# Performance work log

Hardware: AMD Instinct MI355X
Metric: run time of the kernel (lower is better)

## Reference

```python
import jax, jax.numpy as jnp
import numpy as np

NUM_QUERIES = 256
NUM_NEGATIVES = 512
NUM_GENERALIZED = 8
GEN_RADIUS = 1.0
TEMP = 0.5
STRONG_THRESHOLD = 0.97


def _mls(mu0, mu1, s0, s1):
    # mutual likelihood score; mu's are L2-normalized (F.normalize, eps=1e-12)
    mu0 = mu0 / jnp.maximum(jnp.linalg.norm(mu0, axis=-1, keepdims=True), 1e-12)
    mu1 = mu1 / jnp.maximum(jnp.linalg.norm(mu1, axis=-1, keepdims=True), 1e-12)
    down = s0 + s1
    return -0.5 * (((mu0 - mu1) ** 2) / down + jnp.log(down)).mean(-1)


def setup_inputs() -> dict:
    key = jax.random.key(0)
    B, S, H, W, C = 4, 19, 128, 128, 256
    ks = jax.random.split(key, 6)
    mu = jax.random.normal(ks[0], (B, C, H, W), jnp.float32)
    sigma = jax.random.uniform(ks[1], (B, C, H, W), jnp.float32, minval=0.1, maxval=1.0)
    cls = jax.random.randint(ks[2], (B, H, W), 0, S)
    label = jnp.transpose(jax.nn.one_hot(cls, S, dtype=jnp.float32), (0, 3, 1, 2))  # [B,S,H,W]
    mask = jnp.ones((B, 1, H, W), jnp.float32)
    prob = jax.random.uniform(ks[3], (B, S, H, W), jnp.float32)
    mmt_prototype_mu = jax.random.normal(ks[4], (S, 1, C), jnp.float32)
    mmt_prototype_sigma = jax.random.uniform(ks[5], (S, 1, C), jnp.float32, minval=0.1, maxval=1.0)
    return {"mu": mu, "sigma": sigma, "label": label, "mask": mask, "prob": prob,
            "mmt_prototype_mu": mmt_prototype_mu, "mmt_prototype_sigma": mmt_prototype_sigma,
            "epoch": 0, "iter_i": 0}


def reference(mu, sigma, label, mask, prob, mmt_prototype_mu, mmt_prototype_sigma, epoch, iter_i):
    B, C, H, W = mu.shape
    S = label.shape[1]
    P = B * H * W
    Q, NEG, G = NUM_QUERIES, NUM_NEGATIVES, NUM_GENERALIZED
    key = jax.random.key(1234)

    valid = (label * mask).transpose(1, 0, 2, 3).reshape(S, P)            # [S,P] float
    mu_f = mu.transpose(0, 2, 3, 1).reshape(P, C)                          # [P,C]
    sg_f = sigma.transpose(0, 2, 3, 1).reshape(P, C)
    prob_f = prob.transpose(1, 0, 2, 3).reshape(S, P)
    hard = (prob_f < STRONG_THRESHOLD).astype(valid.dtype) * valid         # [S,P]

    # --- segment prototypes (precision-weighted fusion), detached as in torch.no_grad ---
    inv_sg = 1.0 / sg_f
    proto_sigma_b = 1.0 / jnp.einsum('sp,pc->sc', valid, inv_sg)           # [S,C]
    proto_mu_b = proto_sigma_b * jnp.einsum('sp,pc->sc', valid, inv_sg * mu_f)
    mmt_mu = mmt_prototype_mu[:, 0, :]
    mmt_sg = mmt_prototype_sigma[:, 0, :]
    proto_sigma = 1.0 / (1.0 / proto_sigma_b + 1.0 / mmt_sg)               # momentum fusion
    proto_mu = proto_sigma * (mmt_mu / mmt_sg + proto_mu_b / proto_sigma_b)
    proto_mu = jax.lax.stop_gradient(proto_mu)
    proto_sigma = jax.lax.stop_gradient(proto_sigma)

    # cumulative masks for uniform sampling over valid / hard pixels via searchsorted
    valid_cum = jnp.cumsum(valid, axis=1)                                  # [S,P]
    valid_cnt = valid_cum[:, -1]
    hard_cum = jnp.cumsum(hard, axis=1)
    hard_cnt = hard_cum[:, -1]

    loss = jnp.float32(0.0)
    for i in range(S):
        ki = jax.random.fold_in(key, i)
        k_anc, k_cls, k_neg, k_gen = jax.random.split(ki, 4)
        # anchors: uniform over hard pixels of segment i
        u = jax.random.uniform(k_anc, (Q,)) * hard_cnt[i]
        a_idx = jnp.clip(jnp.searchsorted(hard_cum[i], u, side='right'), 0, P - 1)
        anchor_mu = mu_f[a_idx]                                            # [Q,C]
        anchor_sg = sg_f[a_idx]
        # negative class distribution from prototype MLS similarity
        others = jnp.concatenate([jnp.arange(i + 1, S), jnp.arange(0, i)])  # [S-1]
        sim = _mls(proto_mu[i][None], proto_mu[others], proto_sigma[i][None], proto_sigma[others])
        logp = jax.nn.log_softmax(sim / TEMP)
        samp = jax.random.categorical(k_cls, logp, shape=(Q, NEG))          # idx into `others`
        cls_g = others[samp.reshape(-1)]                                    # [Q*NEG] global class
        # uniform pixel within each sampled class (vectorized searchsorted over classes)
        un = jax.random.uniform(k_neg, (Q * NEG,))
        idx_all = jax.vmap(lambda cs, cnt: jnp.searchsorted(cs, un * cnt, side='right'))(valid_cum, valid_cnt)
        n_idx = jnp.clip(idx_all[cls_g, jnp.arange(Q * NEG)], 0, P - 1)
        neg_mu = jax.lax.stop_gradient(mu_f[n_idx].reshape(Q, NEG, C))
        neg_sg = jax.lax.stop_gradient(sg_f[n_idx].reshape(Q, NEG, C))
        pos_mu = jnp.broadcast_to(proto_mu[i][None, None], (Q, 1, C))
        pos_sg = jnp.broadcast_to(proto_sigma[i][None, None], (Q, 1, C))
        # generalized negatives: reparameterized samples from (updated) momentum prototypes
        eps = jax.random.normal(k_gen, (S - 1, G, C))
        gen = proto_mu[others][:, None, :] + GEN_RADIUS * jnp.sqrt(proto_sigma[others])[:, None, :] * eps
        gen = jnp.broadcast_to(gen.reshape(1, (S - 1) * G, C), (Q, (S - 1) * G, C))
        all_mu = jnp.concatenate([pos_mu, neg_mu, gen], axis=1)             # [Q,1+NEG+(S-1)*G,C]
        all_sg = jnp.concatenate([pos_sg, neg_sg, jnp.zeros_like(gen)], axis=1)
        logits = _mls(anchor_mu[:, None, :], all_mu, anchor_sg[:, None, :], all_sg) / TEMP
        loss = loss - jax.nn.log_softmax(logits, axis=-1)[:, 0].mean()      # CE vs target 0
    return loss / S
```

## Files before the change

kernel.cpp:

```cpp
#include <hip/hip_runtime.h>
#include <hip/hip_fp16.h>
#include <hip/hip_fp8.h>
#include <cstdint>

#define B_   4
#define S_   19
#define HW_  16384
#define P_   65536
#define C_   256
#define Q_   256
#define NEG_ 512
#define NS_  131072
#define GENV_ 144
#define NANCH (S_ * 256)
#define NPAIR (NANCH / 2)
#define NBUCK 8

typedef float v2f __attribute__((ext_vector_type(2)));

#if __has_builtin(__builtin_amdgcn_cvt_pk_f32_fp8) && __has_builtin(__builtin_amdgcn_cvt_pk_fp8_f32)
#define HAVE_HW_FP8 1
#endif

template<int W> __device__ __forceinline__ v2f cvt8(uint32_t d) {
#ifdef HAVE_HW_FP8
  v2f r = __builtin_amdgcn_cvt_pk_f32_fp8((int)d, W);
  return r;
#else
  __hip_fp8_e4m3 h0, h1;
  h0.__x = (uint8_t)(d >> (W * 16));
  h1.__x = (uint8_t)(d >> (W * 16 + 8));
  v2f r; r.x = (float)h0; r.y = (float)h1; return r;
#endif
}
template<int W> __device__ __forceinline__ uint32_t pk8(float a, float b, uint32_t old) {
#ifdef HAVE_HW_FP8
  return (uint32_t)__builtin_amdgcn_cvt_pk_fp8_f32(a, b, (int)old, W);
#else
  __hip_fp8_e4m3 ha(a), hb(b);
  uint32_t v = (uint32_t)ha.__x | ((uint32_t)hb.__x << 8);
  return (old & (W ? 0x0000FFFFu : 0xFFFF0000u)) | (v << (W * 16));
#endif
}

__device__ __forceinline__ void tf2x32(uint32_t k0, uint32_t k1, uint32_t x0, uint32_t x1,
                                       uint32_t& o0, uint32_t& o1) {
  uint32_t k2 = k0 ^ k1 ^ 0x1BD11BDAu;
#define TFR(r) { x0 += x1; x1 = (x1 << r) | (x1 >> (32 - r)); x1 ^= x0; }
  x0 += k0; x1 += k1;
  TFR(13) TFR(15) TFR(26) TFR(6)  x0 += k1; x1 += k2 + 1u;
  TFR(17) TFR(29) TFR(16) TFR(24) x0 += k2; x1 += k0 + 2u;
  TFR(13) TFR(15) TFR(26) TFR(6)  x0 += k0; x1 += k1 + 3u;
  TFR(17) TFR(29) TFR(16) TFR(24) x0 += k1; x1 += k2 + 4u;
  TFR(13) TFR(15) TFR(26) TFR(6)  x0 += k2; x1 += k0 + 5u;
#undef TFR
  o0 = x0; o1 = x1;
}

__device__ __forceinline__ uint32_t rbits(uint32_t k0, uint32_t k1, uint32_t n) {
  uint32_t a, b; tf2x32(k0, k1, 0u, n, a, b); return a ^ b;
}

__device__ __forceinline__ float bits2f01(uint32_t b) {
  return __uint_as_float((b >> 9) | 0x3f800000u) - 1.0f;
}

__device__ __forceinline__ float fastrcp(float x) {
  float r; asm("v_rcp_f32 %0, %1" : "=v"(r) : "v"(x)); return r;
}

__device__ __forceinline__ float wred(float v) {
#pragma unroll
  for (int off = 32; off > 0; off >>= 1) v += __shfl_xor(v, off, 64);
  return v;
}
__device__ __forceinline__ void wred3(float& a, float& b, float& c) {
#pragma unroll
  for (int off = 32; off > 0; off >>= 1) {
    a += __shfl_xor(a, off, 64);
    b += __shfl_xor(b, off, 64);
    c += __shfl_xor(c, off, 64);
  }
}

__device__ __forceinline__ void lse_up(float lg, float& m, float& l) {
  if (lg > m) { l = l * __expf(m - lg) + 1.0f; m = lg; }
  else l += __expf(lg - m);
}
__device__ __forceinline__ void lse_merge(float& m, float& l, float mo, float lo) {
  float mn = fmaxf(m, mo);
  l = l * __expf(m - mn) + lo * __expf(mo - mn);
  m = mn;
}

__device__ __forceinline__ float erfinv_f(float x) {
  float w = -__logf(fmaxf(fmaf(-x, x, 1.0f), 1e-37f));
  float p;
  if (w < 5.0f) {
    w -= 2.5f;
    p = 2.81022636e-08f;
    p = fmaf(p, w, 3.43273939e-07f);
    p = fmaf(p, w, -3.5233877e-06f);
    p = fmaf(p, w, -4.39150654e-06f);
    p = fmaf(p, w, 0.00021858087f);
    p = fmaf(p, w, -0.00125372503f);
    p = fmaf(p, w, -0.00417768164f);
    p = fmaf(p, w, 0.246640727f);
    p = fmaf(p, w, 1.50140941f);
  } else {
    w = sqrtf(w) - 3.0f;
    p = -0.000200214257f;
    p = fmaf(p, w, 0.000100950558f);
    p = fmaf(p, w, 0.00134934322f);
    p = fmaf(p, w, -0.00367342844f);
    p = fmaf(p, w, 0.00573950773f);
    p = fmaf(p, w, -0.0076224613f);
    p = fmaf(p, w, 0.00943887047f);
    p = fmaf(p, w, 1.00167406f);
    p = fmaf(p, w, 2.83297682f);
  }
  return p * x;
}

__global__ __launch_bounds__(256) void k_classify(const float* __restrict__ label,
    const float* __restrict__ mask, const float* __restrict__ prob,
    const float* __restrict__ mu,
    uint32_t* __restrict__ keys, int* __restrict__ cls, int* __restrict__ hrd,
    int* __restrict__ bcv, int* __restrict__ bch, float2* __restrict__ rnrm) {
  __shared__ int hv[S_], hh[S_];
  int t = threadIdx.x;
  if (t < S_) { hv[t] = 0; hh[t] = 0; }
  if (blockIdx.x == 0 && t < S_) {
    uint32_t f0, f1;
    tf2x32(0u, 1234u, 0u, (uint32_t)t, f0, f1);
#pragma unroll
    for (int k = 0; k < 4; ++k) {
      uint32_t a, b;
      tf2x32(f0, f1, 0u, (uint32_t)k, a, b);
      keys[t * 8 + k * 2] = a; keys[t * 8 + k * 2 + 1] = b;
    }
  }
  __syncthreads();
  int p = blockIdx.x * 256 + t;
  int b = p >> 14, rem = p & (HW_ - 1);
  int sp = -1;
#pragma unroll
  for (int s = 0; s < S_; ++s) {
    float l = label[((b * S_ + s) << 14) + rem];
    if (l > 0.5f) sp = s;
  }
  if (mask[(b << 14) + rem] <= 0.5f) sp = -1;
  int h = 0;
  if (sp >= 0) h = (prob[((b * S_ + sp) << 14) + rem] < 0.97f) ? 1 : 0;
  cls[p] = sp; hrd[p] = h;
  if (sp >= 0) { atomicAdd(&hv[sp], 1); if (h) atomicAdd(&hh[sp], 1); }
  __syncthreads();
  if (t < S_) { bcv[t * 256 + blockIdx.x] = hv[t]; bch[t * 256 + blockIdx.x] = hh[t]; }
  const float* basep = mu + (((size_t)(b * C_)) << 14) + rem;
  float s2 = 0.f;
#pragma unroll 8
  for (int c = 0; c < C_; ++c) {
    float v = basep[(size_t)c << 14];
    s2 = fmaf(v, v, s2);
  }
  float nrm = sqrtf(s2);
  rnrm[p] = make_float2(fastrcp(fmaxf(nrm, 1e-12f)), nrm);
}

__global__ __launch_bounds__(256) void k_pack(const float* __restrict__ mu,
    const float* __restrict__ sg, const float2* __restrict__ rnrm,
    uint32_t* __restrict__ pair8) {
  __shared__ float smu[64][65];
  __shared__ float ssg[64][65];
  __shared__ float srn[64];
  int p0 = blockIdx.x * 64, c0 = blockIdx.y * 64;
  int b = p0 >> 14, rem0 = p0 & (HW_ - 1);
  if (threadIdx.x < 64) srn[threadIdx.x] = rnrm[p0 + threadIdx.x].x;
  int px = threadIdx.x & 63, cy = threadIdx.x >> 6;
#pragma unroll
  for (int itr = 0; itr < 16; ++itr) {
    int cl = cy + itr * 4;
    int addr = ((b * C_ + c0 + cl) << 14) + rem0 + px;
    smu[cl][px] = mu[addr];
    ssg[cl][px] = sg[addr];
  }
  __syncthreads();
#pragma unroll
  for (int itr = 0; itr < 8; ++itr) {
    int e = itr * 256 + threadIdx.x;
    int pxl = e >> 5, dw = e & 31, cl = dw * 2;
    float rn = srn[pxl];
    uint32_t wd = pk8<0>(smu[cl][pxl] * rn, ssg[cl][pxl], 0u);
    wd = pk8<1>(smu[cl + 1][pxl] * rn, ssg[cl + 1][pxl], wd);
    pair8[(size_t)(p0 + pxl) * 128 + (c0 >> 1) + dw] = wd;
  }
}

__global__ __launch_bounds__(320) void k_scan(const int* __restrict__ bcv, const int* __restrict__ bch,
    int* __restrict__ bov, int* __restrict__ boh,
    int* __restrict__ cntv, int* __restrict__ cnth,
    int* __restrict__ basev, int* __restrict__ baseh) {
  __shared__ int psv[S_][16], psh[S_][16], scv[S_], sch[S_];
  int t = threadIdx.x;
  int s = t >> 4, c = t & 15;
  if (t < 304) {
    int sv = 0, sh = 0;
#pragma unroll 4
    for (int b = 0; b < 16; ++b) {
      sv += bcv[s * 256 + c * 16 + b];
      sh += bch[s * 256 + c * 16 + b];
    }
    psv[s][c] = sv; psh[s][c] = sh;
  }
  __syncthreads();
  if (t < S_) {
    int rv = 0, rh = 0;
#pragma unroll
    for (int cc = 0; cc < 16; ++cc) {
      int tv = psv[t][cc]; psv[t][cc] = rv; rv += tv;
      int th = psh[t][cc]; psh[t][cc] = rh; rh += th;
    }
    cntv[t] = rv; cnth[t] = rh; scv[t] = rv; sch[t] = rh;
  }
  __syncthreads();
  if (t == 0) {
    int bv = 0, bh = 0;
    for (int k = 0; k < S_; ++k) { basev[k] = bv; bv += scv[k]; baseh[k] = bh; bh += sch[k]; }
  }
  if (t < 304) {
    int rv = psv[s][c], rh = psh[s][c];
#pragma unroll 4
    for (int b = 0; b < 16; ++b) {
      int i0 = s * 256 + c * 16 + b;
      int tv = bcv[i0]; bov[i0] = rv; rv += tv;
      int th = bch[i0]; boh[i0] = rh; rh += th;
    }
  }
}

__global__ __launch_bounds__(256) void k_fillsums(const uint32_t* __restrict__ pair8,
    const float2* __restrict__ rnrm, const int* __restrict__ cls, const int* __restrict__ hrd,
    const int* __restrict__ bov, const int* __restrict__ boh,
    const int* __restrict__ basev, const int* __restrict__ baseh,
    int* __restrict__ posv, int* __restrict__ posh, float* __restrict__ part) {
  __shared__ float lacc[S_][2][C_];
  __shared__ int scls[256];
  __shared__ int slh[256];
  __shared__ float snrm[256];
  int t = threadIdx.x;
  int p0 = blockIdx.x * 256;
  int p = p0 + t;
  int s = cls[p]; int h = hrd[p];
  scls[t] = s; slh[t] = h;
  snrm[t] = rnrm[p].y;
  for (int e = t; e < S_ * 2 * C_; e += 256) (&lacc[0][0][0])[e] = 0.f;
  __syncthreads();
  if (s >= 0) {
    int rv = 0, rh = 0;
    for (int k = 0; k < t; ++k) { if (scls[k] == s) { rv++; rh += slh[k]; } }
    posv[basev[s] + bov[s * 256 + blockIdx.x] + rv] = p;
    if (h) posh[baseh[s] + boh[s * 256 + blockIdx.x] + rh] = p;
  }
  int half = t & 1, dwi = t >> 1;
  uint32_t d = pair8[(size_t)p0 * 128 + dwi];
  for (int pp = 0; pp < 256; ++pp) {
    uint32_t dnx = (pp + 1 < 256) ? pair8[(size_t)(p0 + pp + 1) * 128 + dwi] : 0u;
    int sc = scls[pp];
    if (sc >= 0) {
      v2f e = half ? cvt8<1>(d) : cvt8<0>(d);
      float ia = fastrcp(e.y);
      lacc[sc][0][t] += ia;
      lacc[sc][1][t] += ia * e.x * snrm[pp];
    }
    d = dnx;
  }
  __syncthreads();
  float* dst = part + (size_t)blockIdx.x * (2 * S_ * C_);
  for (int e = t; e < S_ * 2 * C_; e += 256) dst[e] = (&lacc[0][0][0])[e];
}

__global__ __launch_bounds__(1024) void k_proto(const float* __restrict__ part,
    const float* __restrict__ mmu, const float* __restrict__ msg,
    float* __restrict__ pmu, float* __restrict__ psig, float* __restrict__ phat) {
  __shared__ float redA[4][C_];
  __shared__ float redB[4][C_];
  __shared__ float red[4];
  int s = blockIdx.x;
  int t = threadIdx.x;
  int c = t & 255, grp = t >> 8;
  float A = 0.f, Bv = 0.f;
  for (int b = grp * 64; b < grp * 64 + 64; ++b) {
    const float* pb = part + (size_t)b * (2 * S_ * C_) + (s * 2) * C_;
    A += pb[c];
    Bv += pb[C_ + c];
  }
  redA[grp][c] = A; redB[grp][c] = Bv;
  __syncthreads();
  float pm = 0.f;
  if (grp == 0) {
    A = redA[0][c] + redA[1][c] + redA[2][c] + redA[3][c];
    Bv = redB[0][c] + redB[1][c] + redB[2][c] + redB[3][c];
    int e = s * C_ + c;
    float psb = 1.0f / A;
    float pmb = psb * Bv;
    float ms = msg[e], mm = mmu[e];
    float ps = 1.0f / (1.0f / psb + 1.0f / ms);
    pm = ps * (mm / ms + pmb / psb);
    pmu[e] = pm; psig[e] = ps;
    float w = wred(pm * pm);
    int lane = c & 63, wv = c >> 6;
    if (lane == 0) red[wv] = w;
  }
  __syncthreads();
  if (grp == 0) {
    float tot = red[0] + red[1] + red[2] + red[3];
    float nrm = fmaxf(sqrtf(tot), 1e-12f);
    phat[s * C_ + c] = pm / nrm;
  }
}

__global__ __launch_bounds__(64) void k_simlogp(const float* __restrict__ phat,
    const float* __restrict__ psig, float* __restrict__ logp) {
  int i = blockIdx.x, lane = threadIdx.x;
  int c0 = lane * 4;
  float phi[4], psi[4];
#pragma unroll
  for (int k = 0; k < 4; ++k) { phi[k] = phat[i * C_ + c0 + k]; psi[k] = psig[i * C_ + c0 + k]; }
  float xs[18];
#pragma unroll
  for (int j = 0; j < 18; ++j) {
    int o = i + 1 + j; if (o >= S_) o -= S_;
    float t = 0.f;
#pragma unroll
    for (int k = 0; k < 4; ++k) {
      float d = phi[k] - phat[o * C_ + c0 + k];
      float dn = psi[k] + psig[o * C_ + c0 + k];
      t += d * d / dn + logf(dn);
    }
    t = wred(t);
    xs[j] = (-0.5f * t * (1.0f / 256.0f)) * 2.0f;
  }
  float m = xs[0];
#pragma unroll
  for (int j = 1; j < 18; ++j) m = fmaxf(m, xs[j]);
  float se = 0.f;
#pragma unroll
  for (int j = 0; j < 18; ++j) se += expf(xs[j] - m);
  float lg = logf(se);
  if (lane == 0) {
#pragma unroll
    for (int j = 0; j < 18; ++j) logp[i * 18 + j] = xs[j] - m - lg;
  }
}

__global__ __launch_bounds__(256) void k_gensample(const uint32_t* __restrict__ keys,
    const float* __restrict__ pmu, const float* __restrict__ psig,
    const float* __restrict__ logp, const int* __restrict__ cntv, const int* __restrict__ basev,
    const int* __restrict__ posv, float* __restrict__ ghat, int* __restrict__ nidx) {
  __shared__ float red[4];
  __shared__ float elp[18];
  __shared__ int lcnt[S_], lbase[S_];
  int bid = blockIdx.x;
  int t = threadIdx.x;
  if (bid < GENV_ * S_) {
    int v = bid % GENV_, i = bid / GENV_;
    int c = t;
    int o = i + 1 + (v >> 3); if (o >= S_) o -= S_;
    uint32_t k0 = keys[i * 8 + 6], k1 = keys[i * 8 + 7];
    uint32_t bits = rbits(k0, k1, (uint32_t)(v * C_ + c));
    float f01 = bits2f01(bits);
    const float lo = -0.99999994f;
    float u = fmaxf(f01 * 2.0f + lo, lo);
    float eps = 1.41421356237f * erfinv_f(u);
    float g = pmu[o * C_ + c] + sqrtf(psig[o * C_ + c]) * eps;
    float w = wred(g * g);
    int lane = c & 63, wv = c >> 6;
    if (lane == 0) red[wv] = w;
    __syncthreads();
    float tot = red[0] + red[1] + red[2] + red[3];
    float nrm = fmaxf(sqrtf(tot), 1e-12f);
    ghat[((size_t)(i * GENV_ + v)) * C_ + c] = g / nrm;
  } else {
    int sid = bid - GENV_ * S_;
    int i = sid / 512;
    int m = (sid % 512) * 256 + t;
    if (t < 18) elp[t] = __expf(-logp[i * 18 + t]);
    if (t < S_) { lcnt[t] = cntv[t]; lbase[t] = basev[t]; }
    __syncthreads();
    uint32_t kc0 = keys[i * 8 + 2], kc1 = keys[i * 8 + 3];
    uint32_t kn0 = keys[i * 8 + 4], kn1 = keys[i * 8 + 5];
    float bv = 1e30f; int best = 0;
    for (int s = 0; s < 18; ++s) {
      uint32_t b = rbits(kc0, kc1, (uint32_t)m * 18u + (uint32_t)s);
      float u = fmaxf(bits2f01(b), 1.17549435e-38f);
      float val = (-__logf(u)) * elp[s];
      if (val < bv) { bv = val; best = s; }
    }
    float un = bits2f01(rbits(kn0, kn1, (uint32_t)m));
    int cc = i + 1 + best; if (cc >= S_) cc -= S_;
    int cnt = lcnt[cc];
    int idx = P_ - 1;
    if (cnt > 0) {
      int kk = (int)(un * (float)cnt);
      if (kk >= cnt) kk = cnt - 1;
      idx = posv[lbase[cc] + kk];
    }
    nidx[(size_t)i * NS_ + m] = idx;
  }
}

__global__ __launch_bounds__(64) void k_bucket(const uint32_t* __restrict__ keys,
    const int* __restrict__ cnth, const int* __restrict__ baseh, const int* __restrict__ posh,
    const int* __restrict__ nidx, int* __restrict__ snidx, int* __restrict__ boff,
    int* __restrict__ aidx) {
  int a = blockIdx.x;
  int lane = threadIdx.x;
  if (lane == 0) {
    int i = a >> 8, q = a & 255;
    uint32_t k0 = keys[i * 8 + 0], k1 = keys[i * 8 + 1];
    float u = bits2f01(rbits(k0, k1, (uint32_t)q));
    int cnt = cnth[i];
    int idx = P_ - 1;
    if (cnt > 0) {
      int kk = (int)(u * (float)cnt);
      if (kk >= cnt) kk = cnt - 1;
      idx = posh[baseh[i] + kk];
    }
    aidx[a] = idx;
  }
  const int* src = nidx + (size_t)a * NEG_;
  int e[8], bk[8];
#pragma unroll
  for (int c = 0; c < 8; ++c) { e[c] = src[c * 64 + lane]; bk[c] = (e[c] >> 13) & 7; }
  uint32_t cnt[NBUCK];
#pragma unroll
  for (int b = 0; b < NBUCK; ++b) cnt[b] = 0;
#pragma unroll
  for (int c = 0; c < 8; ++c)
#pragma unroll
    for (int b = 0; b < NBUCK; ++b) {
      unsigned long long mb = __ballot(bk[c] == b);
      cnt[b] += (uint32_t)__popcll(mb);
    }
  uint32_t base[NBUCK]; uint32_t run = 0;
#pragma unroll
  for (int b = 0; b < NBUCK; ++b) { base[b] = run; run += cnt[b]; }
  if (lane < NBUCK) boff[a * 9 + lane] = (int)base[lane];
  if (lane == 0) boff[a * 9 + 8] = NEG_;
  uint32_t off[NBUCK];
#pragma unroll
  for (int b = 0; b < NBUCK; ++b) off[b] = 0;
  unsigned long long ltm = (1ull << lane) - 1ull;
#pragma unroll
  for (int c = 0; c < 8; ++c) {
    int pos = 0;
#pragma unroll
    for (int b = 0; b < NBUCK; ++b) {
      unsigned long long mb = __ballot(bk[c] == b);
      if (bk[c] == b) pos = (int)(base[b] + off[b] + (uint32_t)__popcll(mb & ltm));
      off[b] += (uint32_t)__popcll(mb);
    }
    snidx[(size_t)a * NEG_ + pos] = e[c];
  }
}

__global__ __launch_bounds__(64) void k_neg(const uint32_t* __restrict__ pair8,
    const int* __restrict__ snidx, const int* __restrict__ boff,
    const int* __restrict__ aidx, float2* __restrict__ partial) {
  __shared__ float4 anc[260];
  int bid = blockIdx.x;
  int bucket = bid & 7;
  int pr = bid >> 3;
  int a0 = pr * 2, a1 = a0 + 1;
  int lane = threadIdx.x;

  int ap0 = aidx[a0], ap1 = aidx[a1];
  uint2 d0 = ((const uint2*)(pair8 + (size_t)ap0 * 128))[lane];
  uint2 d1 = ((const uint2*)(pair8 + (size_t)ap1 * 128))[lane];
  {
    v2f ex = cvt8<0>(d0.x), ey = cvt8<1>(d0.x), ez = cvt8<0>(d0.y), ew = cvt8<1>(d0.y);
    anc[lane * 2]     = make_float4(ex.x, ex.y, ey.x, ey.y);
    anc[lane * 2 + 1] = make_float4(ez.x, ez.y, ew.x, ew.y);
    ex = cvt8<0>(d1.x); ey = cvt8<1>(d1.x); ez = cvt8<0>(d1.y); ew = cvt8<1>(d1.y);
    anc[130 + lane * 2]     = make_float4(ex.x, ex.y, ey.x, ey.y);
    anc[130 + lane * 2 + 1] = make_float4(ez.x, ez.y, ew.x, ew.y);
  }
  __syncthreads();

  int s0 = boff[a0 * 9 + bucket], e0i = boff[a0 * 9 + bucket + 1];
  int s1 = boff[a1 * 9 + bucket], e1i = boff[a1 * 9 + bucket + 1];
  int L0 = e0i - s0, L1 = e1i - s1, Lt = L0 + L1;
  const int* list0 = snidx + (size_t)a0 * NEG_ + s0;
  const int* list1 = snidx + (size_t)a1 * NEG_ + s1;

  float m0 = -1e30f, l0 = 0.f, m1 = -1e30f, l1 = 0.f;

  for (int r = 0; r * 64 < Lt; ++r) {
    int g = r * 64 + lane;
    bool act = g < Lt;
    int which = (act && g >= L0) ? 1 : 0;
    int j = which ? (g - L0) : g;
    int p = act ? (which ? list1[j] : list0[j]) : ap0;
    const uint4* rp = (const uint4*)(pair8 + (size_t)p * 128);
    const float4* A = anc + which * 130;
    float sT = 0.f, sL = 0.f;
    uint4 c0 = rp[0], c1 = rp[1];
#pragma unroll 1
    for (int it = 0; it < 16; ++it) {
      int nx = ((it + 1) & 15) * 2;
      uint4 n0 = rp[nx], n1 = rp[nx + 1];
      uint32_t dws[8] = {c0.x, c0.y, c0.z, c0.w, c1.x, c1.y, c1.z, c1.w};
      float pp = 1.0f, pq = 1.0f;
#pragma unroll
      for (int gq = 0; gq < 4; ++gq) {
        float4 acA = A[it * 8 + gq * 2];
        float4 acB = A[it * 8 + gq * 2 + 1];
        v2f e0v = cvt8<0>(dws[2 * gq]),     e1v = cvt8<1>(dws[2 * gq]);
        v2f e2v = cvt8<0>(dws[2 * gq + 1]), e3v = cvt8<1>(dws[2 * gq + 1]);
        float dn0 = acA.y + e0v.y, dn1 = acA.w + e1v.y;
        float dn2 = acB.y + e2v.y, dn3 = acB.w + e3v.y;
        float d01 = dn0 * dn1, d23 = dn2 * dn3;
        float R01 = fastrcp(d01), R23 = fastrcp(d23);
        pp *= d01; pq *= d23;
        float r0 = dn1 * R01, r1 = dn0 * R01, r2 = dn3 * R23, r3 = dn2 * R23;
        float f0 = acA.x - e0v.x, f1 = acA.z - e1v.x;
        float f2 = acB.x - e2v.x, f3 = acB.z - e3v.x;
        sT = fmaf(f0 * f0, r0, sT); sT = fmaf(f1 * f1, r1, sT);
        sT = fmaf(f2 * f2, r2, sT); sT = fmaf(f3 * f3, r3, sT);
      }
      sL += __logf(pp * pq);
      c0 = n0; c1 = n1;
    }
    float lg = -(sT + sL) * (1.0f / 256.0f);
    if (act) { if (which) lse_up(lg, m1, l1); else lse_up(lg, m0, l0); }
  }
#pragma unroll
  for (int o = 32; o > 0; o >>= 1) {
    float mo = __shfl_xor(m0, o, 64), lo = __shfl_xor(l0, o, 64);
    lse_merge(m0, l0, mo, lo);
    mo = __shfl_xor(m1, o, 64); lo = __shfl_xor(l1, o, 64);
    lse_merge(m1, l1, mo, lo);
  }
  if (lane == 0) {
    partial[a0 * NBUCK + bucket] = make_float2(m0, l0);
    partial[a1 * NBUCK + bucket] = make_float2(m1, l1);
  }
}

__global__ __launch_bounds__(256, 4) void k_fin(const uint32_t* __restrict__ pair8,
    const float* __restrict__ phat, const float* __restrict__ psig,
    const float* __restrict__ ghat, const int* __restrict__ aidx,
    const float2* __restrict__ partial, float* __restrict__ out) {
  __shared__ float2 ancG[C_];
  __shared__ float redm[3][4];
  __shared__ float2 mlw[4];

  int bid = blockIdx.x;
  int i = bid >> 8;
  int t = threadIdx.x, w = t >> 6, lane = t & 63;

  int ap = aidx[bid];
  uint32_t ad = pair8[(size_t)ap * 128 + (t >> 1)];
  v2f ae0 = cvt8<0>(ad), ae1 = cvt8<1>(ad);
  float ahat = (t & 1) ? ae1.x : ae0.x;
  float asg = (t & 1) ? ae1.y : ae0.y;
  float wv = fastrcp(asg);
  ancG[t] = make_float2(wv, ahat * wv);

  float pm = phat[i * C_ + t];
  float ps = psig[i * C_ + t];
  float dnp = asg + ps;
  float dd = ahat - pm;
  float post = fmaf(dd * dd, fastrcp(dnp), __logf(dnp));
  float a1t = ahat * ahat * wv;
  float lat = __logf(asg);
  wred3(post, a1t, lat);
  if (lane == 0) { redm[0][w] = post; redm[1][w] = a1t; redm[2][w] = lat; }
  __syncthreads();
  float postS = redm[0][0] + redm[0][1] + redm[0][2] + redm[0][3];
  float Kc = (redm[1][0] + redm[1][1] + redm[1][2] + redm[1][3])
           + (redm[2][0] + redm[2][1] + redm[2][2] + redm[2][3]);
  float logit0 = -postS * (1.0f / 256.0f);

  float m = -1e30f, l = 0.0f;
  const float4* ancGf = (const float4*)ancG;
  if (lane < 36) {
    int g = lane * 4 + w;
    const float4* gp = (const float4*)(ghat + ((size_t)(i * GENV_ + g)) * C_);
    float a1 = 0.f, a2 = 0.f;
    for (int itr = 0; itr < 64; ++itr) {
      float4 gv = gp[itr];
      float4 g01 = ancGf[itr * 2];
      float4 g23 = ancGf[itr * 2 + 1];
      a1 = fmaf(gv.x * gv.x, g01.x, a1); a2 = fmaf(gv.x, g01.y, a2);
      a1 = fmaf(gv.y * gv.y, g01.z, a1); a2 = fmaf(gv.y, g01.w, a2);
      a1 = fmaf(gv.z * gv.z, g23.x, a1); a2 = fmaf(gv.z, g23.y, a2);
      a1 = fmaf(gv.w * gv.w, g23.z, a1); a2 = fmaf(gv.w, g23.w, a2);
    }
    float lg = -(Kc + a1 - 2.0f * a2) * (1.0f / 256.0f);
    lse_up(lg, m, l);
  }
#pragma unroll
  for (int o = 32; o > 0; o >>= 1) {
    float mo = __shfl_xor(m, o, 64);
    float lo = __shfl_xor(l, o, 64);
    lse_merge(m, l, mo, lo);
  }
  if (lane == 0) mlw[w] = make_float2(m, l);
  __syncthreads();
  if (t == 0) {
    float mm = mlw[0].x, ll = mlw[0].y;
    lse_merge(mm, ll, mlw[1].x, mlw[1].y);
    lse_merge(mm, ll, mlw[2].x, mlw[2].y);
    lse_merge(mm, ll, mlw[3].x, mlw[3].y);
    const float2* pp = partial + (size_t)bid * NBUCK;
#pragma unroll
    for (int b = 0; b < NBUCK; ++b) lse_merge(mm, ll, pp[b].x, pp[b].y);
    lse_merge(mm, ll, logit0, 1.0f);
    float lse = mm + __logf(ll);
    float contrib = logit0 - lse;
    atomicAdd(out, -contrib * (1.0f / (19.0f * 256.0f)));
  }
}

extern "C" void kernel_launch(void* const* d_in, const int* in_sizes, int n_in,
                              void* d_out, int out_size, void* d_ws, size_t ws_size,
                              hipStream_t stream) {
  const float* mu    = (const float*)d_in[0];
  const float* sg    = (const float*)d_in[1];
  const float* label = (const float*)d_in[2];
  const float* mask  = (const float*)d_in[3];
  const float* prob  = (const float*)d_in[4];
  const float* mmu   = (const float*)d_in[5];
  const float* msg   = (const float*)d_in[6];

  char* ws = (char*)d_ws;
  size_t off = 0;
  auto take = [&](size_t bytes) { size_t r = off; off = (off + bytes + 255) & ~(size_t)255; return r; };
  size_t o_pair8 = take((size_t)P_ * 128 * 4);
  size_t o_rnrm  = take((size_t)P_ * 8);
  size_t o_cls   = take((size_t)P_ * 4);
  size_t o_hrd   = take((size_t)P_ * 4);
  size_t o_bcv   = take(S_ * 256 * 4);
  size_t o_bch   = take(S_ * 256 * 4);
  size_t o_bov   = take(S_ * 256 * 4);
  size_t o_boh   = take(S_ * 256 * 4);
  size_t o_cntv  = take(S_ * 4);
  size_t o_cnth  = take(S_ * 4);
  size_t o_basev = take(S_ * 4);
  size_t o_baseh = take(S_ * 4);
  size_t o_posv  = take((size_t)P_ * 4);
  size_t o_posh  = take((size_t)P_ * 4);
  size_t o_part  = take((size_t)256 * 2 * S_ * C_ * 4);
  size_t o_pmu   = take(S_ * C_ * 4);
  size_t o_psig  = take(S_ * C_ * 4);
  size_t o_phat  = take(S_ * C_ * 4);
  size_t o_logp  = take(S_ * 18 * 4);
  size_t o_keys  = take(S_ * 8 * 4);
  size_t o_aidx  = take(S_ * Q_ * 4);
  size_t o_nidx  = take((size_t)S_ * NS_ * 4);
  size_t o_snidx = take((size_t)S_ * NS_ * 4);
  size_t o_boff  = take((size_t)NANCH * 9 * 4);
  size_t o_lpar  = take((size_t)NANCH * NBUCK * 8);
  size_t o_ghat  = take((size_t)S_ * GENV_ * C_ * 4);
  if (ws_size < off) return;

  uint32_t* pair8 = (uint32_t*)(ws + o_pair8);
  float2*   rnrm  = (float2*)(ws + o_rnrm);
  int*      cls   = (int*)(ws + o_cls);
  int*      hrd   = (int*)(ws + o_hrd);
  int*      bcv   = (int*)(ws + o_bcv);
  int*      bch   = (int*)(ws + o_bch);
  int*      bov   = (int*)(ws + o_bov);
  int*      boh   = (int*)(ws + o_boh);
  int*      cntv  = (int*)(ws + o_cntv);
  int*      cnth  = (int*)(ws + o_cnth);
  int*      basev = (int*)(ws + o_basev);
  int*      baseh = (int*)(ws + o_baseh);
  int*      posv  = (int*)(ws + o_posv);
  int*      posh  = (int*)(ws + o_posh);
  float*    part  = (float*)(ws + o_part);
  float*    pmu   = (float*)(ws + o_pmu);
  float*    psig  = (float*)(ws + o_psig);
  float*    phat  = (float*)(ws + o_phat);
  float*    logp  = (float*)(ws + o_logp);
  uint32_t* keys  = (uint32_t*)(ws + o_keys);
  int*      aidx  = (int*)(ws + o_aidx);
  int*      nidx  = (int*)(ws + o_nidx);
  int*      snidx = (int*)(ws + o_snidx);
  int*      boff  = (int*)(ws + o_boff);
  float2*   lpar  = (float2*)(ws + o_lpar);
  float*    ghat  = (float*)(ws + o_ghat);

  hipMemsetAsync(d_out, 0, (size_t)out_size * 4, stream);

  k_classify<<<256, 256, 0, stream>>>(label, mask, prob, mu, keys, cls, hrd, bcv, bch, rnrm);
  k_pack<<<dim3(P_ / 64, C_ / 64), 256, 0, stream>>>(mu, sg, rnrm, pair8);
  k_scan<<<1, 320, 0, stream>>>(bcv, bch, bov, boh, cntv, cnth, basev, baseh);
  k_fillsums<<<256, 256, 0, stream>>>(pair8, rnrm, cls, hrd, bov, boh, basev, baseh, posv, posh, part);
  k_proto<<<S_, 1024, 0, stream>>>(part, mmu, msg, pmu, psig, phat);
  k_simlogp<<<S_, 64, 0, stream>>>(phat, psig, logp);
  k_gensample<<<GENV_ * S_ + 512 * S_, 256, 0, stream>>>(keys, pmu, psig, logp, cntv, basev, posv, ghat, nidx);
  k_bucket<<<NANCH, 64, 0, stream>>>(keys, cnth, baseh, posh, nidx, snidx, boff, aidx);
  k_neg<<<NBUCK * NPAIR, 64, 0, stream>>>(pair8, snidx, boff, aidx, lpar);
  k_fin<<<NANCH, 256, 0, stream>>>(pair8, phat, psig, ghat, aidx, lpar, (float*)d_out);
}
```

Measured before the change: 604.1 us.

## Pack four anchors per k_neg wavefront and use ballot-based rank in fillsums

k_neg now processes four anchors per 64-lane block instead of two. This packs the bucket lists more densely across lanes so fewer lanes sit idle in the final partial round, and it halves the number of blocks. k_fillsums replaces an O(t) serial shared-memory scan for within-block rank with per-class wavefront ballots plus per-wave prefix counts. The trade-offs are more registers for four LSE accumulators, more shared memory for the anchors, and fewer blocks to fill the GPU.

```diff
diff --git a/kernel.cpp b/kernel.cpp
--- a/kernel.cpp
+++ b/kernel.cpp
@@ -13,7 +13,6 @@
 #define NS_  131072
 #define GENV_ 144
 #define NANCH (S_ * 256)
-#define NPAIR (NANCH / 2)
 #define NBUCK 8
 
 typedef float v2f __attribute__((ext_vector_type(2)));
@@ -245,19 +244,29 @@
     int* __restrict__ posv, int* __restrict__ posh, float* __restrict__ part) {
   __shared__ float lacc[S_][2][C_];
   __shared__ int scls[256];
-  __shared__ int slh[256];
   __shared__ float snrm[256];
+  __shared__ int cntW[4][S_], cnthW[4][S_];
   int t = threadIdx.x;
+  int w = t >> 6, lane = t & 63;
   int p0 = blockIdx.x * 256;
   int p = p0 + t;
   int s = cls[p]; int h = hrd[p];
-  scls[t] = s; slh[t] = h;
+  scls[t] = s;
   snrm[t] = rnrm[p].y;
   for (int e = t; e < S_ * 2 * C_; e += 256) (&lacc[0][0][0])[e] = 0.f;
+  unsigned long long ltm = (1ull << lane) - 1ull;
+  unsigned long long mv = 0ull, mh = 0ull;
+  for (int sc = 0; sc < S_; ++sc) {
+    unsigned long long mb = __ballot(s == sc);
+    unsigned long long mbh = __ballot(s == sc && h);
+    if (s == sc) { mv = mb; mh = mbh; }
+    if (lane == 0) { cntW[w][sc] = (int)__popcll(mb); cnthW[w][sc] = (int)__popcll(mbh); }
+  }
   __syncthreads();
   if (s >= 0) {
-    int rv = 0, rh = 0;
-    for (int k = 0; k < t; ++k) { if (scls[k] == s) { rv++; rh += slh[k]; } }
+    int rv = (int)__popcll(mv & ltm);
+    int rh = (int)__popcll(mh & ltm);
+    for (int w2 = 0; w2 < w; ++w2) { rv += cntW[w2][s]; rh += cnthW[w2][s]; }
     posv[basev[s] + bov[s * 256 + blockIdx.x] + rv] = p;
     if (h) posh[baseh[s] + boh[s * 256 + blockIdx.x] + rh] = p;
   }
@@ -467,42 +476,59 @@
 __global__ __launch_bounds__(64) void k_neg(const uint32_t* __restrict__ pair8,
     const int* __restrict__ snidx, const int* __restrict__ boff,
     const int* __restrict__ aidx, float2* __restrict__ partial) {
-  __shared__ float4 anc[260];
+  __shared__ float4 anc[4][130];
   int bid = blockIdx.x;
   int bucket = bid & 7;
   int pr = bid >> 3;
-  int a0 = pr * 2, a1 = a0 + 1;
+  int a0 = pr * 4;
   int lane = threadIdx.x;
 
-  int ap0 = aidx[a0], ap1 = aidx[a1];
-  uint2 d0 = ((const uint2*)(pair8 + (size_t)ap0 * 128))[lane];
-  uint2 d1 = ((const uint2*)(pair8 + (size_t)ap1 * 128))[lane];
+  int apx = aidx[a0 + 0], apy = aidx[a0 + 1], apz = aidx[a0 + 2], apw = aidx[a0 + 3];
   {
-    v2f ex = cvt8<0>(d0.x), ey = cvt8<1>(d0.x), ez = cvt8<0>(d0.y), ew = cvt8<1>(d0.y);
-    anc[lane * 2]     = make_float4(ex.x, ex.y, ey.x, ey.y);
-    anc[lane * 2 + 1] = make_float4(ez.x, ez.y, ew.x, ew.y);
-    ex = cvt8<0>(d1.x); ey = cvt8<1>(d1.x); ez = cvt8<0>(d1.y); ew = cvt8<1>(d1.y);
-    anc[130 + lane * 2]     = make_float4(ex.x, ex.y, ey.x, ey.y);
-    anc[130 + lane * 2 + 1] = make_float4(ez.x, ez.y, ew.x, ew.y);
-  }
-  __syncthreads();
-
-  int s0 = boff[a0 * 9 + bucket], e0i = boff[a0 * 9 + bucket + 1];
-  int s1 = boff[a1 * 9 + bucket], e1i = boff[a1 * 9 + bucket + 1];
-  int L0 = e0i - s0, L1 = e1i - s1, Lt = L0 + L1;
-  const int* list0 = snidx + (size_t)a0 * NEG_ + s0;
-  const int* list1 = snidx + (size_t)a1 * NEG_ + s1;
-
-  float m0 = -1e30f, l0 = 0.f, m1 = -1e30f, l1 = 0.f;
+    uint2 d = ((const uint2*)(pair8 + (size_t)apx * 128))[lane];
+    v2f ex = cvt8<0>(d.x), ey = cvt8<1>(d.x), ez = cvt8<0>(d.y), ew = cvt8<1>(d.y);
+    anc[0][lane * 2]     = make_float4(ex.x, ex.y, ey.x, ey.y);
+    anc[0][lane * 2 + 1] = make_float4(ez.x, ez.y, ew.x, ew.y);
+    d = ((const uint2*)(pair8 + (size_t)apy * 128))[lane];
+    ex = cvt8<0>(d.x); ey = cvt8<1>(d.x); ez = cvt8<0>(d.y); ew = cvt8<1>(d.y);
+    anc[1][lane * 2]     = make_float4(ex.x, ex.y, ey.x, ey.y);
+    anc[1][lane * 2 + 1] = make_float4(ez.x, ez.y, ew.x, ew.y);
+    d = ((const uint2*)(pair8 + (size_t)apz * 128))[lane];
+    ex = cvt8<0>(d.x); ey = cvt8<1>(d.x); ez = cvt8<0>(d.y); ew = cvt8<1>(d.y);
+    anc[2][lane * 2]     = make_float4(ex.x, ex.y, ey.x, ey.y);
+    anc[2][lane * 2 + 1] = make_float4(ez.x, ez.y, ew.x, ew.y);
+    d = ((const uint2*)(pair8 + (size_t)apw * 128))[lane];
+    ex = cvt8<0>(d.x); ey = cvt8<1>(d.x); ez = cvt8<0>(d.y); ew = cvt8<1>(d.y);
+    anc[3][lane * 2]     = make_float4(ex.x, ex.y, ey.x, ey.y);
+    anc[3][lane * 2 + 1] = make_float4(ez.x, ez.y, ew.x, ew.y);
+  }
+  __syncthreads();
+
+  int s0 = boff[(a0 + 0) * 9 + bucket], e0 = boff[(a0 + 0) * 9 + bucket + 1];
+  int s1 = boff[(a0 + 1) * 9 + bucket], e1 = boff[(a0 + 1) * 9 + bucket + 1];
+  int s2 = boff[(a0 + 2) * 9 + bucket], e2 = boff[(a0 + 2) * 9 + bucket + 1];
+  int s3 = boff[(a0 + 3) * 9 + bucket], e3 = boff[(a0 + 3) * 9 + bucket + 1];
+  int L0 = e0 - s0, L1 = e1 - s1, L2 = e2 - s2, L3 = e3 - s3;
+  int c01 = L0 + L1, c012 = c01 + L2, Lt = c012 + L3;
+  const int* lst0 = snidx + (size_t)(a0 + 0) * NEG_ + s0;
+  const int* lst1 = snidx + (size_t)(a0 + 1) * NEG_ + s1;
+  const int* lst2 = snidx + (size_t)(a0 + 2) * NEG_ + s2;
+  const int* lst3 = snidx + (size_t)(a0 + 3) * NEG_ + s3;
+
+  float m0 = -1e30f, l0v = 0.f, m1 = -1e30f, l1v = 0.f;
+  float m2 = -1e30f, l2v = 0.f, m3 = -1e30f, l3v = 0.f;
 
   for (int r = 0; r * 64 < Lt; ++r) {
     int g = r * 64 + lane;
     bool act = g < Lt;
-    int which = (act && g >= L0) ? 1 : 0;
-    int j = which ? (g - L0) : g;
-    int p = act ? (which ? list1[j] : list0[j]) : ap0;
+    int which = (g >= L0) + (g >= c01) + (g >= c012);
+    if (!act) which = 0;
+    int sub = (which == 0) ? 0 : (which == 1) ? L0 : (which == 2) ? c01 : c012;
+    int j = g - sub;
+    const int* lp = (which == 0) ? lst0 : (which == 1) ? lst1 : (which == 2) ? lst2 : lst3;
+    int p = act ? lp[j] : apx;
     const uint4* rp = (const uint4*)(pair8 + (size_t)p * 128);
-    const float4* A = anc + which * 130;
+    const float4* A = anc[which];
     float sT = 0.f, sL = 0.f;
     uint4 c0 = rp[0], c1 = rp[1];
 #pragma unroll 1
@@ -532,18 +558,26 @@
       c0 = n0; c1 = n1;
     }
     float lg = -(sT + sL) * (1.0f / 256.0f);
-    if (act) { if (which) lse_up(lg, m1, l1); else lse_up(lg, m0, l0); }
+    if (act) {
+      if (which == 0) lse_up(lg, m0, l0v);
+      else if (which == 1) lse_up(lg, m1, l1v);
+      else if (which == 2) lse_up(lg, m2, l2v);
+      else lse_up(lg, m3, l3v);
+    }
   }
 #pragma unroll
   for (int o = 32; o > 0; o >>= 1) {
-    float mo = __shfl_xor(m0, o, 64), lo = __shfl_xor(l0, o, 64);
-    lse_merge(m0, l0, mo, lo);
-    mo = __shfl_xor(m1, o, 64); lo = __shfl_xor(l1, o, 64);
-    lse_merge(m1, l1, mo, lo);
+    float mo, lo;
+    mo = __shfl_xor(m0, o, 64); lo = __shfl_xor(l0v, o, 64); lse_merge(m0, l0v, mo, lo);
+    mo = __shfl_xor(m1, o, 64); lo = __shfl_xor(l1v, o, 64); lse_merge(m1, l1v, mo, lo);
+    mo = __shfl_xor(m2, o, 64); lo = __shfl_xor(l2v, o, 64); lse_merge(m2, l2v, mo, lo);
+    mo = __shfl_xor(m3, o, 64); lo = __shfl_xor(l3v, o, 64); lse_merge(m3, l3v, mo, lo);
   }
   if (lane == 0) {
-    partial[a0 * NBUCK + bucket] = make_float2(m0, l0);
-    partial[a1 * NBUCK + bucket] = make_float2(m1, l1);
+    partial[(a0 + 0) * NBUCK + bucket] = make_float2(m0, l0v);
+    partial[(a0 + 1) * NBUCK + bucket] = make_float2(m1, l1v);
+    partial[(a0 + 2) * NBUCK + bucket] = make_float2(m2, l2v);
+    partial[(a0 + 3) * NBUCK + bucket] = make_float2(m3, l3v);
   }
 }
 
@@ -702,6 +736,6 @@
   k_simlogp<<<S_, 64, 0, stream>>>(phat, psig, logp);
   k_gensample<<<GENV_ * S_ + 512 * S_, 256, 0, stream>>>(keys, pmu, psig, logp, cntv, basev, posv, ghat, nidx);
   k_bucket<<<NANCH, 64, 0, stream>>>(keys, cnth, baseh, posh, nidx, snidx, boff, aidx);
-  k_neg<<<NBUCK * NPAIR, 64, 0, stream>>>(pair8, snidx, boff, aidx, lpar);
+  k_neg<<<NBUCK * (NANCH / 4), 64, 0, stream>>>(pair8, snidx, boff, aidx, lpar);
   k_fin<<<NANCH, 256, 0, stream>>>(pair8, phat, psig, ghat, aidx, lpar, (float*)d_out);
 }
```

Result: faster. 586.7 us (-2.9%).
